# Performance work log

Measured on AMD Instinct MI355X. Metric: run time of the kernel, lower is better.

The kernel has to match this reference:

```python
import jax, jax.numpy as jnp
import numpy as np
from jax import lax

B, S, I, H, L = 2, 1024, 1024, 1024, 2


def setup_inputs() -> dict:
    key = jax.random.key(0)
    ks = jax.random.split(key, 8)
    scale = 0.02
    return {
        "embeddings": jax.random.normal(ks[0], (B, S, I), dtype=jnp.float32),
        "W_r": jax.random.normal(ks[1], (L, H, I + H), dtype=jnp.float32) * scale,
        "b_r": jnp.zeros((L, H), dtype=jnp.float32),
        "W_z": jax.random.normal(ks[2], (L, H, I + H), dtype=jnp.float32) * scale,
        "b_z": jnp.zeros((L, H), dtype=jnp.float32),
        "W_h": jax.random.normal(ks[3], (L, H, I + H), dtype=jnp.float32) * scale,
        "b_h": jnp.zeros((L, H), dtype=jnp.float32),
    }


def _run_gru(embeddings, W_r, b_r, W_z, b_z, W_h, b_h):
    # The source iterates embeddings[i][j] with ONE shared hidden vector,
    # i.e. the flattened batch*seq stream is processed sequentially.
    x_flat = embeddings.reshape(-1, embeddings.shape[-1])  # [B*S, I]
    h = jnp.zeros((H,), dtype=embeddings.dtype)
    n_layers = W_r.shape[0]
    for l in range(n_layers):  # small fixed layer loop; each layer is a distinct param set
        Wr, br = W_r[l], b_r[l]
        Wz, bz = W_z[l], b_z[l]
        Wh, bh = W_h[l], b_h[l]

        def step(h, x):
            hx = jnp.concatenate([h, x])           # [H + I]
            r = jax.nn.sigmoid(Wr @ hx + br)       # [H]
            z = jax.nn.sigmoid(Wz @ hx + bz)       # [H]
            hh = jnp.tanh(Wh @ jnp.concatenate([r * h, x]) + bh)
            h_new = (1.0 - z) * h + z * hh
            return h_new, None

        h, _ = lax.scan(step, h, x_flat)
        # MyGRU passes the previous layer's final hidden as the next layer's
        # initial hidden, and re-feeds the original embeddings.
    return h


def reference(embeddings, W_r, b_r, W_z, b_z, W_h, b_h):
    h = _run_gru(embeddings, W_r, b_r, W_z, b_z, W_h, b_h)
    return (h, h)  # (output, hidden) -- identical in the source
```

## Files before the change

### kernel.cpp

```cpp
#include <hip/hip_runtime.h>
#include <hip/hip_cooperative_groups.h>

constexpr int HD    = 1024;
constexpr int SEQ   = 2048;
constexpr int NL    = 2;
constexpr int NSTEP = NL * SEQ;
constexpr int NBLK  = 32;
constexpr int TPB   = 512;
constexpr int RPC   = 32;
constexpr int KPT   = 64;
constexpr int NMIR  = 8;

typedef unsigned u32x4 __attribute__((ext_vector_type(4)));

__device__ __forceinline__ unsigned packbf(float v, unsigned tag) {
  unsigned b = __float_as_uint(v);
  b += 0x7FFFu + ((b >> 16) & 1u);
  return (tag << 16) | (b >> 16);
}
__device__ __forceinline__ unsigned pack2(float a, float b) {
  unsigned ua = __float_as_uint(a); ua += 0x7FFFu + ((ua >> 16) & 1u);
  unsigned ub = __float_as_uint(b); ub += 0x7FFFu + ((ub >> 16) & 1u);
  return (ua >> 16) | (ub & 0xFFFF0000u);
}
__device__ __forceinline__ bool tags_ok(u32x4 v, unsigned tag) {
  return (v.x >> 16) == tag && (v.y >> 16) == tag &&
         (v.z >> 16) == tag && (v.w >> 16) == tag;
}
__device__ __forceinline__ u32x4 poll4(const unsigned* p, unsigned tag) {
  u32x4 a, b;
  asm volatile("s_waitcnt vmcnt(0)" ::: "memory");
  asm volatile("global_load_dwordx4 %0, %1, off sc0 sc1"
               : "=&v"(a) : "v"(p) : "memory");
  while (true) {
    asm volatile("global_load_dwordx4 %0, %1, off sc0 sc1\n\t"
                 "s_waitcnt vmcnt(1)"
                 : "=&v"(b) : "v"(p) : "memory");
    __builtin_amdgcn_sched_barrier(0);
    if (tags_ok(a, tag)) {
      asm volatile("s_waitcnt vmcnt(0)" ::: "memory");
      return a;
    }
    asm volatile("global_load_dwordx4 %0, %1, off sc0 sc1\n\t"
                 "s_waitcnt vmcnt(1)"
                 : "=&v"(a) : "v"(p) : "memory");
    __builtin_amdgcn_sched_barrier(0);
    if (tags_ok(b, tag)) {
      asm volatile("s_waitcnt vmcnt(0)" ::: "memory");
      return b;
    }
  }
}
__device__ __forceinline__ void wave_publish(unsigned* base, unsigned wv,
                                             int lane, int pubrow) {
  const unsigned w0 = __shfl(wv, 0);
  const unsigned w1 = __shfl(wv, 16);
  const unsigned w2 = __shfl(wv, 32);
  const unsigned w3 = __shfl(wv, 48);
  if (lane < NMIR) {
    u32x4 o; o.x = w0; o.y = w1; o.z = w2; o.w = w3;
    unsigned* dst = base + lane * HD + pubrow;
    asm volatile("global_store_dwordx4 %0, %1, off sc0 sc1"
                 :: "v"(dst), "v"(o) : "memory");
  }
}
__device__ __forceinline__ void load_gate(const float* p, unsigned (&dst)[32]) {
#pragma unroll
  for (int j = 0; j < 16; ++j) {
    const float4 v = *reinterpret_cast<const float4*>(p + 4 * j);
    dst[2 * j]     = pack2(v.x, v.y);
    dst[2 * j + 1] = pack2(v.z, v.w);
  }
}
__device__ __forceinline__ float red16(float s) {
  s += __shfl_xor(s, 8, 16);
  s += __shfl_xor(s, 4, 16);
  s += __shfl_xor(s, 2, 16);
  s += __shfl_xor(s, 1, 16);
  return s;
}
__device__ __forceinline__ int swz(int lp) { return lp + (lp >> 5); }
constexpr int SLDS = 16 * 33;

__global__ void __launch_bounds__(256) ax_gemm_kernel(
    const float* __restrict__ X,
    const float* __restrict__ Wr, const float* __restrict__ Wz, const float* __restrict__ Wh,
    const float* __restrict__ br, const float* __restrict__ bz, const float* __restrict__ bh,
    float* __restrict__ ax)
{
  __shared__ float sX[16][64];
  __shared__ float sW[16][64];

  const int gl = blockIdx.z, l = gl / 3, g = gl % 3;
  const float* W    = (g == 0 ? Wr : (g == 1 ? Wz : Wh)) + (size_t)l * HD * (2 * HD) + HD;
  const float* bias = (g == 0 ? br : (g == 1 ? bz : bh)) + l * HD;
  const int t0 = blockIdx.y * 64, r0 = blockIdx.x * 64;
  const int tid = threadIdx.x;
  const int tx = tid & 15;
  const int ty = tid >> 4;
  const int lt = tid >> 2;
  const int lk = (tid & 3) * 4;

  float acc[4][4] = {};

  for (int k0 = 0; k0 < HD; k0 += 16) {
    float4 xv = *reinterpret_cast<const float4*>(&X[(size_t)(t0 + lt) * HD + k0 + lk]);
    float4 wv = *reinterpret_cast<const float4*>(&W[(size_t)(r0 + lt) * (2 * HD) + k0 + lk]);
    __syncthreads();
    sX[lk + 0][lt] = xv.x; sX[lk + 1][lt] = xv.y; sX[lk + 2][lt] = xv.z; sX[lk + 3][lt] = xv.w;
    sW[lk + 0][lt] = wv.x; sW[lk + 1][lt] = wv.y; sW[lk + 2][lt] = wv.z; sW[lk + 3][lt] = wv.w;
    __syncthreads();
#pragma unroll
    for (int k = 0; k < 16; ++k) {
      float4 a = *reinterpret_cast<const float4*>(&sX[k][ty * 4]);
      float4 b = *reinterpret_cast<const float4*>(&sW[k][tx * 4]);
      const float av[4] = {a.x, a.y, a.z, a.w};
      const float bv[4] = {b.x, b.y, b.z, b.w};
#pragma unroll
      for (int i = 0; i < 4; ++i)
#pragma unroll
        for (int j = 0; j < 4; ++j)
          acc[i][j] += av[i] * bv[j];
    }
  }

  float4 bb = *reinterpret_cast<const float4*>(&bias[r0 + tx * 4]);
  const float bv[4] = {bb.x, bb.y, bb.z, bb.w};
#pragma unroll
  for (int i = 0; i < 4; ++i) {
    float4 o;
    o.x = acc[i][0] + bv[0]; o.y = acc[i][1] + bv[1];
    o.z = acc[i][2] + bv[2]; o.w = acc[i][3] + bv[3];
    *reinterpret_cast<float4*>(
        &ax[((size_t)gl * SEQ + t0 + ty * 4 + i) * HD + r0 + tx * 4]) = o;
  }
}

__global__ void __launch_bounds__(TPB) gru_seq_kernel(
    const float* __restrict__ Wr, const float* __restrict__ Wz, const float* __restrict__ Wh,
    const float* __restrict__ ax,
    unsigned* __restrict__ hpack, unsigned* __restrict__ rhpack,
    float* __restrict__ outp)
{
  __shared__ unsigned sH[SLDS];
  __shared__ unsigned sRH[SLDS];

  const int wg   = blockIdx.x;
  const int tid  = threadIdx.x;
  const int rloc = tid >> 4;
  const int grow = wg * RPC + rloc;
  const int kcIdx = tid & 15;
  const int kc   = kcIdx * KPT;
  const int lane = tid & 63;
  const int wave = tid >> 6;
  const int pubrow = wg * RPC + wave * 4;
  const bool lead = (kcIdx == 0);
  const int mymir = (wg & (NMIR - 1)) * HD;

  unsigned wr_[32], wz_[32], wh_[32];
  auto load_layer = [&](int l) {
    const size_t off = ((size_t)l * HD + grow) * (size_t)(2 * HD) + kc;
    load_gate(Wr + off, wr_);
    load_gate(Wz + off, wz_);
    load_gate(Wh + off, wh_);
  };
  load_layer(0);

  float hreg = 0.0f;
  float zv = 0.0f;
  float axr  = ax[(size_t)0 * SEQ * HD + grow];
  float axz  = ax[(size_t)1 * SEQ * HD + grow];
  float axh_ = ax[(size_t)2 * SEQ * HD + grow];

  for (int u = 0; u < NSTEP; ++u) {
    if (u == SEQ) load_layer(1);
    const int pb  = (u & 1) * NMIR * HD;
    const int pbn = ((u + 1) & 1) * NMIR * HD;

    if (tid < 256) {
      u32x4 v = poll4(&hpack[pb + mymir + 4 * tid], (unsigned)u);
      const int lp = 2 * tid;
      sH[swz(lp)]     = (v.y << 16) | (v.x & 0xFFFFu);
      sH[swz(lp + 1)] = (v.w << 16) | (v.z & 0xFFFFu);
    }
    __syncthreads();
    {
      const unsigned* hp = &sH[kcIdx * 33];
      float sr = 0.0f;
#pragma unroll
      for (int m = 0; m < 32; ++m) {
        const unsigned hpair = hp[m];
        const unsigned a = wr_[m];
        sr = fmaf(__uint_as_float(a << 16), __uint_as_float(hpair << 16), sr);
        sr = fmaf(__uint_as_float(a & 0xFFFF0000u),
                  __uint_as_float(hpair & 0xFFFF0000u), sr);
      }
      sr = red16(sr);
      const float rg = 1.0f / (1.0f + expf(-(sr + axr)));
      wave_publish(rhpack + pb, packbf(rg * hreg, (unsigned)(u + 1)),
                   lane, pubrow);
      float sz = 0.0f;
#pragma unroll
      for (int m = 0; m < 32; ++m) {
        const unsigned hpair = hp[m];
        const unsigned b = wz_[m];
        sz = fmaf(__uint_as_float(b << 16), __uint_as_float(hpair << 16), sz);
        sz = fmaf(__uint_as_float(b & 0xFFFF0000u),
                  __uint_as_float(hpair & 0xFFFF0000u), sz);
      }
      sz = red16(sz);
      zv = 1.0f / (1.0f + expf(-(sz + axz)));
    }

    if (tid < 256) {
      u32x4 v = poll4(&rhpack[pb + mymir + 4 * tid], (unsigned)(u + 1));
      const int lp = 2 * tid;
      sRH[swz(lp)]     = (v.y << 16) | (v.x & 0xFFFFu);
      sRH[swz(lp + 1)] = (v.w << 16) | (v.z & 0xFFFFu);
    }
    __syncthreads();
    {
      const unsigned* rp = &sRH[kcIdx * 33];
      float sh = 0.0f;
#pragma unroll
      for (int m = 0; m < 32; ++m) {
        const unsigned rpair = rp[m];
        const unsigned c = wh_[m];
        sh = fmaf(__uint_as_float(c << 16), __uint_as_float(rpair << 16), sh);
        sh = fmaf(__uint_as_float(c & 0xFFFF0000u),
                  __uint_as_float(rpair & 0xFFFF0000u), sh);
      }
      sh = red16(sh);
      const float hh = tanhf(sh + axh_);
      const float hn = (1.0f - zv) * hreg + zv * hh;
      hreg = hn;
      wave_publish(hpack + pbn, packbf(hn, (unsigned)(u + 1)), lane, pubrow);
      if (u == NSTEP - 1 && lead) {
        outp[grow] = hn;
        outp[HD + grow] = hn;
      }
      const int un = (u + 1 < NSTEP) ? u + 1 : u;
      const int ln = un >> 11, tn = un & (SEQ - 1);
      axr  = ax[(((size_t)ln * 3 + 0) * SEQ + tn) * HD + grow];
      axz  = ax[(((size_t)ln * 3 + 1) * SEQ + tn) * HD + grow];
      axh_ = ax[(((size_t)ln * 3 + 2) * SEQ + tn) * HD + grow];
    }
  }
}

extern "C" void kernel_launch(void* const* d_in, const int* in_sizes, int n_in,
                              void* d_out, int out_size, void* d_ws, size_t ws_size,
                              hipStream_t stream) {
  const float* emb = (const float*)d_in[0];
  const float* Wr  = (const float*)d_in[1];
  const float* br  = (const float*)d_in[2];
  const float* Wz  = (const float*)d_in[3];
  const float* bz  = (const float*)d_in[4];
  const float* Wh  = (const float*)d_in[5];
  const float* bh  = (const float*)d_in[6];
  float* outp = (float*)d_out;

  float*    ws     = (float*)d_ws;
  float*    ax     = ws;
  unsigned* hpack  = (unsigned*)(ws + (size_t)6 * SEQ * HD);
  unsigned* rhpack = hpack + 2 * NMIR * HD;

  hipMemsetAsync(hpack, 0, 4 * NMIR * HD * sizeof(unsigned), stream);

  dim3 g1(HD / 64, SEQ / 64, 6);
  ax_gemm_kernel<<<g1, 256, 0, stream>>>(emb, Wr, Wz, Wh, br, bz, bh, ax);

  void* args[] = {(void*)&Wr, (void*)&Wz, (void*)&Wh, (void*)&ax,
                  (void*)&hpack, (void*)&rhpack, (void*)&outp};
  hipLaunchCooperativeKernel((const void*)gru_seq_kernel, dim3(NBLK), dim3(TPB),
                             args, 0, stream);
}
```

Baseline: 14.58 ms.

## Use dedicated producer waves with LDS flag handshakes instead of block barriers

Adds four extra waves per block that poll the global h and r*h buffers and fill shared memory, signalling readiness through workgroup-scope atomic counters. The compute waves wait on these counters instead of __syncthreads, and acknowledge consumption so the producers can overwrite the buffers. This is meant to overlap the global polling with the matvec compute and to take block-wide barriers off the serial per-step critical path. It also removes the leading vmcnt wait in poll4. The cost is more threads per block and spin-waiting on LDS counters, which adds ordering risk.

```diff
diff --git a/kernel.cpp b/kernel.cpp
--- a/kernel.cpp
+++ b/kernel.cpp
@@ -6,7 +6,8 @@
 constexpr int NL    = 2;
 constexpr int NSTEP = NL * SEQ;
 constexpr int NBLK  = 32;
-constexpr int TPB   = 512;
+constexpr int TPB   = 768;
+constexpr int CTH   = 512;
 constexpr int RPC   = 32;
 constexpr int KPT   = 64;
 constexpr int NMIR  = 8;
@@ -29,7 +30,6 @@
 }
 __device__ __forceinline__ u32x4 poll4(const unsigned* p, unsigned tag) {
   u32x4 a, b;
-  asm volatile("s_waitcnt vmcnt(0)" ::: "memory");
   asm volatile("global_load_dwordx4 %0, %1, off sc0 sc1"
                : "=&v"(a) : "v"(p) : "memory");
   while (true) {
@@ -79,6 +79,13 @@
   s += __shfl_xor(s, 1, 16);
   return s;
 }
+__device__ __forceinline__ void lds_wait(int* p, int target) {
+  while (__hip_atomic_load(p, __ATOMIC_ACQUIRE, __HIP_MEMORY_SCOPE_WORKGROUP)
+         < target) {}
+}
+__device__ __forceinline__ void lds_bump(int* p) {
+  __hip_atomic_fetch_add(p, 1, __ATOMIC_RELEASE, __HIP_MEMORY_SCOPE_WORKGROUP);
+}
 __device__ __forceinline__ int swz(int lp) { return lp + (lp >> 5); }
 constexpr int SLDS = 16 * 33;
 
@@ -144,9 +151,35 @@
 {
   __shared__ unsigned sH[SLDS];
   __shared__ unsigned sRH[SLDS];
-
-  const int wg   = blockIdx.x;
-  const int tid  = threadIdx.x;
+  __shared__ int sHReady, sRHReady, sHAck, sRHAck;
+
+  const int wg  = blockIdx.x;
+  const int tid = threadIdx.x;
+  const int mymir = (wg & (NMIR - 1)) * HD;
+
+  if (tid == 0) { sHReady = 0; sRHReady = 0; sHAck = 0; sRHAck = 0; }
+  __syncthreads();
+
+  if (tid >= CTH) {
+    const int p = tid - CTH;
+    const bool wlead = ((tid & 63) == 0);
+    const int lp = 2 * p;
+    for (int u = 0; u < NSTEP; ++u) {
+      const int pb = (u & 1) * NMIR * HD;
+      u32x4 v = poll4(&hpack[pb + mymir + 4 * p], (unsigned)u);
+      lds_wait(&sHAck, 8 * u);
+      sH[swz(lp)]     = (v.y << 16) | (v.x & 0xFFFFu);
+      sH[swz(lp + 1)] = (v.w << 16) | (v.z & 0xFFFFu);
+      if (wlead) lds_bump(&sHReady);
+      v = poll4(&rhpack[pb + mymir + 4 * p], (unsigned)(u + 1));
+      lds_wait(&sRHAck, 8 * u);
+      sRH[swz(lp)]     = (v.y << 16) | (v.x & 0xFFFFu);
+      sRH[swz(lp + 1)] = (v.w << 16) | (v.z & 0xFFFFu);
+      if (wlead) lds_bump(&sRHReady);
+    }
+    return;
+  }
+
   const int rloc = tid >> 4;
   const int grow = wg * RPC + rloc;
   const int kcIdx = tid & 15;
@@ -154,8 +187,8 @@
   const int lane = tid & 63;
   const int wave = tid >> 6;
   const int pubrow = wg * RPC + wave * 4;
-  const bool lead = (kcIdx == 0);
-  const int mymir = (wg & (NMIR - 1)) * HD;
+  const bool alead = (lane == 0);
+  const bool olead = (kcIdx == 0);
 
   unsigned wr_[32], wz_[32], wh_[32];
   auto load_layer = [&](int l) {
@@ -177,13 +210,7 @@
     const int pb  = (u & 1) * NMIR * HD;
     const int pbn = ((u + 1) & 1) * NMIR * HD;
 
-    if (tid < 256) {
-      u32x4 v = poll4(&hpack[pb + mymir + 4 * tid], (unsigned)u);
-      const int lp = 2 * tid;
-      sH[swz(lp)]     = (v.y << 16) | (v.x & 0xFFFFu);
-      sH[swz(lp + 1)] = (v.w << 16) | (v.z & 0xFFFFu);
-    }
-    __syncthreads();
+    lds_wait(&sHReady, 4 * (u + 1));
     {
       const unsigned* hp = &sH[kcIdx * 33];
       float sr = 0.0f;
@@ -210,15 +237,10 @@
       }
       sz = red16(sz);
       zv = 1.0f / (1.0f + expf(-(sz + axz)));
-    }
-
-    if (tid < 256) {
-      u32x4 v = poll4(&rhpack[pb + mymir + 4 * tid], (unsigned)(u + 1));
-      const int lp = 2 * tid;
-      sRH[swz(lp)]     = (v.y << 16) | (v.x & 0xFFFFu);
-      sRH[swz(lp + 1)] = (v.w << 16) | (v.z & 0xFFFFu);
-    }
-    __syncthreads();
+      if (alead) lds_bump(&sHAck);
+    }
+
+    lds_wait(&sRHReady, 4 * (u + 1));
     {
       const unsigned* rp = &sRH[kcIdx * 33];
       float sh = 0.0f;
@@ -235,7 +257,8 @@
       const float hn = (1.0f - zv) * hreg + zv * hh;
       hreg = hn;
       wave_publish(hpack + pbn, packbf(hn, (unsigned)(u + 1)), lane, pubrow);
-      if (u == NSTEP - 1 && lead) {
+      if (alead) lds_bump(&sRHAck);
+      if (u == NSTEP - 1 && olead) {
         outp[grow] = hn;
         outp[HD + grow] = hn;
       }
```

Result: slower. 21.85 ms (+49.9%).
